# Performance work log

Hardware: AMD Instinct MI355X
Metric: run time of the kernel (lower is better)

The kernel has to match this reference:

```python
import jax, jax.numpy as jnp
import numpy as np

N_NODES = 100000
N_EDGES = 1600000
IN_DIM = 64
EMBED_DIM = 128
OUT_DIM = 10


def setup_inputs() -> dict:
    key = jax.random.key(0)
    ks = jax.random.split(key, 12)
    x = jax.random.normal(ks[0], (N_NODES, IN_DIM), dtype=jnp.float32)
    edge_index = jax.random.randint(ks[1], (2, N_EDGES), 0, N_NODES, dtype=jnp.int64)
    s = lambda k, shp, fan_in: jax.random.normal(k, shp, dtype=jnp.float32) / np.sqrt(fan_in)
    # SAGEConv params: lin_l (applied to aggregated neighbors, has bias), lin_r (root, no bias)
    W_l = s(ks[2], (IN_DIM, EMBED_DIM), IN_DIM)
    b_l = jnp.zeros((EMBED_DIM,), dtype=jnp.float32)
    W_r = s(ks[3], (IN_DIM, EMBED_DIM), IN_DIM)
    # Classifier MLP: embed -> 64 -> 128 -> out
    W1 = s(ks[4], (EMBED_DIM, 64), EMBED_DIM)
    b1 = jnp.zeros((64,), dtype=jnp.float32)
    W2 = s(ks[5], (64, 128), 64)
    b2 = jnp.zeros((128,), dtype=jnp.float32)
    W3 = s(ks[6], (128, OUT_DIM), 128)
    b3 = jnp.zeros((OUT_DIM,), dtype=jnp.float32)
    return {"x": x, "edge_index": edge_index, "W_l": W_l, "b_l": b_l, "W_r": W_r,
            "W1": W1, "b1": b1, "W2": W2, "b2": b2, "W3": W3, "b3": b3}


def reference(x, edge_index, W_l, b_l, W_r, W1, b1, W2, b2, W3, b3):
    src, dst = edge_index[0], edge_index[1]
    # mean-aggregate neighbor features: gather x[src], scatter-sum to dst, divide by degree
    msg = x[src]                                                   # [E, in_dim]
    agg = jax.ops.segment_sum(msg, dst, num_segments=N_NODES)      # [N, in_dim]
    deg = jax.ops.segment_sum(jnp.ones((src.shape[0],), x.dtype), dst, num_segments=N_NODES)
    mean = agg / jnp.maximum(deg, 1.0)[:, None]                    # [N, in_dim]
    # SAGEConv: lin_l(mean_neigh) + lin_r(x_root)
    h = mean @ W_l + b_l + x @ W_r                                 # [N, embed_dim]
    # classifier MLP (logits)
    h = jax.nn.relu(h @ W1 + b1)
    h = jax.nn.relu(h @ W2 + b2)
    return h @ W3 + b3
```

## Files before the change

kernel.cpp:

```cpp
#include <hip/hip_runtime.h>
#include <hip/hip_bf16.h>

#define N_NODES 100000
#define IN_DIM 64
#define EMB 128
#define HID1 64
#define HID2 128
#define OUT_DIM 10

#define CHUNK 8192
#define NBUCK ((N_NODES + 511) >> 9)
#define CAPB 9216

using short8 = __attribute__((ext_vector_type(8))) short;
using bfx4   = __attribute__((ext_vector_type(4))) short;
using f32x4  = __attribute__((ext_vector_type(4))) float;

__device__ inline short f2bf(float f) {
  __hip_bfloat16 h = __float2bfloat16(f);
  return *reinterpret_cast<short*>(&h);
}

#define WCAT_N (128 * 128)
#define W1T_N  (64 * 128)
#define W2T_N  (128 * 64)
#define W3T_N  (16 * 128)
__global__ __launch_bounds__(256) void prep_weights(
    const float* __restrict__ W_l, const float* __restrict__ W_r,
    const float* __restrict__ W1, const float* __restrict__ W2,
    const float* __restrict__ W3,
    short* __restrict__ wcat_t, short* __restrict__ w1t,
    short* __restrict__ w2t, short* __restrict__ w3t)
{
  int t = blockIdx.x * 256 + threadIdx.x;
  if (t < WCAT_N) {
    int c = t >> 7, k = t & 127;
    float v = (k < 64) ? W_r[k * EMB + c] : W_l[(k - 64) * EMB + c];
    wcat_t[c * 128 + k] = f2bf(v);
  } else if (t < WCAT_N + W1T_N) {
    int u = t - WCAT_N;
    int c = u >> 7, k = u & 127;
    w1t[c * 128 + k] = f2bf(W1[k * HID1 + c]);
  } else if (t < WCAT_N + W1T_N + W2T_N) {
    int u = t - WCAT_N - W1T_N;
    int c = u >> 6, k = u & 63;
    w2t[c * 64 + k] = f2bf(W2[k * HID2 + c]);
  } else if (t < WCAT_N + W1T_N + W2T_N + W3T_N) {
    int u = t - WCAT_N - W1T_N - W2T_N;
    int c = u >> 7, k = u & 127;
    w3t[c * 128 + k] = (c < OUT_DIM) ? f2bf(W3[k * OUT_DIM + c]) : (short)0;
  }
}

__global__ __launch_bounds__(256) void convert_x(
    const float* __restrict__ x, short* __restrict__ comb)
{
  int t = blockIdx.x * 256 + threadIdx.x;
  if (t >= N_NODES * 16) return;
  int node = t >> 4, g = t & 15;
  f32x4 v = *(const f32x4*)&x[(size_t)node * IN_DIM + g * 4];
  bfx4 s;
#pragma unroll
  for (int i = 0; i < 4; ++i) s[i] = f2bf(v[i]);
  *(bfx4*)&comb[((size_t)node << 7) + g * 4] = s;
}

__global__ __launch_bounds__(256) void bin_scatter(
    const int* __restrict__ src, const int* __restrict__ dst,
    int* __restrict__ gcur, int* __restrict__ ebuf, int E)
{
  __shared__ int hist[NBUCK], excl[NBUCK], cur[NBUCK], gb[NBUCK];
  __shared__ int stage[CHUNK];
  __shared__ unsigned char bof[CHUNK];
  __shared__ int sc[256];
  const int tid = threadIdx.x;
  const int base = blockIdx.x * CHUNK;
  const int cn = min(CHUNK, E - base);

  for (int i = tid; i < NBUCK; i += 256) hist[i] = 0;
  __syncthreads();
  for (int i = tid; i < cn; i += 256) atomicAdd(&hist[dst[base + i] >> 9], 1);
  __syncthreads();

  int v = (tid < NBUCK) ? hist[tid] : 0;
  sc[tid] = v;
  __syncthreads();
  for (int off = 1; off < 256; off <<= 1) {
    int u = (tid >= off) ? sc[tid - off] : 0;
    __syncthreads();
    sc[tid] += u;
    __syncthreads();
  }
  if (tid < NBUCK) {
    int ex = sc[tid] - v;
    excl[tid] = ex; cur[tid] = ex;
    gb[tid] = v ? atomicAdd(&gcur[tid], v) : 0;
  }
  __syncthreads();

  for (int i = tid; i < cn; i += 256) {
    int d = dst[base + i], s = src[base + i];
    int bk = d >> 9;
    int pos = atomicAdd(&cur[bk], 1);
    stage[pos] = ((d & 511) << 17) | s;
    bof[pos] = (unsigned char)bk;
  }
  __syncthreads();

  for (int i = tid; i < cn; i += 256) {
    int bk = bof[i];
    int idx = gb[bk] + (i - excl[bk]);
    if (idx < CAPB) ebuf[bk * CAPB + idx] = stage[i];
  }
}

__global__ __launch_bounds__(256) void bucket_csr(
    const int* __restrict__ gcur, int* __restrict__ ebuf,
    int* __restrict__ offs, int* __restrict__ oend)
{
  __shared__ int cnt[512], cur[512], sc[512];
  __shared__ int ep[CAPB];
  __shared__ int es[CAPB];
  const int b = blockIdx.x, tid = threadIdx.x;
  const int node0 = b << 9;
  const int nn = min(512, N_NODES - node0);
  const int ebase = b * CAPB;
  const int ecnt = min(gcur[b], CAPB);

  for (int i = tid; i < 512; i += 256) cnt[i] = 0;
  __syncthreads();
  for (int i = tid; i < ecnt; i += 256) {
    int p = ebuf[ebase + i];
    ep[i] = p;
    atomicAdd(&cnt[p >> 17], 1);
  }
  __syncthreads();
  for (int i = tid; i < 512; i += 256) sc[i] = cnt[i];
  __syncthreads();
  for (int off = 1; off < 512; off <<= 1) {
    int i0 = tid, i1 = tid + 256;
    int v0 = (i0 >= off) ? sc[i0 - off] : 0;
    int v1 = (i1 >= off) ? sc[i1 - off] : 0;
    __syncthreads();
    sc[i0] += v0; sc[i1] += v1;
    __syncthreads();
  }
  for (int i = tid; i < 512; i += 256) {
    int ex = sc[i] - cnt[i];
    cur[i] = ex;
    if (i < nn) {
      offs[node0 + i] = ebase + ex;
      oend[node0 + i] = ebase + sc[i];
    }
  }
  __syncthreads();
  for (int i = tid; i < ecnt; i += 256) {
    int p = ep[i];
    int pos = atomicAdd(&cur[p >> 17], 1);
    es[pos] = p & 131071;
  }
  __syncthreads();
  for (int i = tid; i < ecnt; i += 256) ebuf[ebase + i] = es[i];
}

__global__ __launch_bounds__(256) void aggregate_kernel(
    const int* __restrict__ offs, const int* __restrict__ oend,
    const int* __restrict__ esrc, short* __restrict__ comb)
{
  int wave = (int)((blockIdx.x * 256 + threadIdx.x) >> 6);
  int lane = threadIdx.x & 63;
  if (wave >= N_NODES) return;
  const int h = lane >> 5, li = lane & 31;
  const int beg = offs[wave], end = oend[wave];
  float a0 = 0.f, a1 = 0.f;

  for (int e = beg; e < end; e += 64) {
    const int cnt = min(end - e, 64);
    int sidx = (lane < cnt) ? esrc[e + lane] : 0;
    int jb = 0;
    for (; jb + 16 <= cnt; jb += 16) {
      int j = jb + h;
      int s0 = __shfl(sidx, j,      64);
      int s1 = __shfl(sidx, j + 2,  64);
      int s2 = __shfl(sidx, j + 4,  64);
      int s3 = __shfl(sidx, j + 6,  64);
      int s4 = __shfl(sidx, j + 8,  64);
      int s5 = __shfl(sidx, j + 10, 64);
      int s6 = __shfl(sidx, j + 12, 64);
      int s7 = __shfl(sidx, j + 14, 64);
      unsigned v0 = *(const unsigned*)&comb[((size_t)s0 << 7) + (li << 1)];
      unsigned v1 = *(const unsigned*)&comb[((size_t)s1 << 7) + (li << 1)];
      unsigned v2 = *(const unsigned*)&comb[((size_t)s2 << 7) + (li << 1)];
      unsigned v3 = *(const unsigned*)&comb[((size_t)s3 << 7) + (li << 1)];
      unsigned v4 = *(const unsigned*)&comb[((size_t)s4 << 7) + (li << 1)];
      unsigned v5 = *(const unsigned*)&comb[((size_t)s5 << 7) + (li << 1)];
      unsigned v6 = *(const unsigned*)&comb[((size_t)s6 << 7) + (li << 1)];
      unsigned v7 = *(const unsigned*)&comb[((size_t)s7 << 7) + (li << 1)];
      a0 += __uint_as_float(v0 << 16); a1 += __uint_as_float(v0 & 0xFFFF0000u);
      a0 += __uint_as_float(v1 << 16); a1 += __uint_as_float(v1 & 0xFFFF0000u);
      a0 += __uint_as_float(v2 << 16); a1 += __uint_as_float(v2 & 0xFFFF0000u);
      a0 += __uint_as_float(v3 << 16); a1 += __uint_as_float(v3 & 0xFFFF0000u);
      a0 += __uint_as_float(v4 << 16); a1 += __uint_as_float(v4 & 0xFFFF0000u);
      a0 += __uint_as_float(v5 << 16); a1 += __uint_as_float(v5 & 0xFFFF0000u);
      a0 += __uint_as_float(v6 << 16); a1 += __uint_as_float(v6 & 0xFFFF0000u);
      a0 += __uint_as_float(v7 << 16); a1 += __uint_as_float(v7 & 0xFFFF0000u);
    }
    if (jb + 8 <= cnt) {
      int j = jb + h;
      int s0 = __shfl(sidx, j,     64);
      int s1 = __shfl(sidx, j + 2, 64);
      int s2 = __shfl(sidx, j + 4, 64);
      int s3 = __shfl(sidx, j + 6, 64);
      unsigned v0 = *(const unsigned*)&comb[((size_t)s0 << 7) + (li << 1)];
      unsigned v1 = *(const unsigned*)&comb[((size_t)s1 << 7) + (li << 1)];
      unsigned v2 = *(const unsigned*)&comb[((size_t)s2 << 7) + (li << 1)];
      unsigned v3 = *(const unsigned*)&comb[((size_t)s3 << 7) + (li << 1)];
      a0 += __uint_as_float(v0 << 16); a1 += __uint_as_float(v0 & 0xFFFF0000u);
      a0 += __uint_as_float(v1 << 16); a1 += __uint_as_float(v1 & 0xFFFF0000u);
      a0 += __uint_as_float(v2 << 16); a1 += __uint_as_float(v2 & 0xFFFF0000u);
      a0 += __uint_as_float(v3 << 16); a1 += __uint_as_float(v3 & 0xFFFF0000u);
      jb += 8;
    }
    for (; jb < cnt; jb += 2) {
      int j = jb + h;
      int s0 = __shfl(sidx, j & 63, 64);
      if (j < cnt) {
        unsigned v0 = *(const unsigned*)&comb[((size_t)s0 << 7) + (li << 1)];
        a0 += __uint_as_float(v0 << 16); a1 += __uint_as_float(v0 & 0xFFFF0000u);
      }
    }
  }
  a0 += __shfl_xor(a0, 32, 64);
  a1 += __shfl_xor(a1, 32, 64);
  if (h == 0) {
    float d = fmaxf((float)(end - beg), 1.0f);
    float m0 = a0 / d, m1 = a1 / d;
    unsigned p = ((unsigned)(unsigned short)f2bf(m1) << 16) |
                 (unsigned short)f2bf(m0);
    *(unsigned*)&comb[((size_t)wave << 7) + 64 + (li << 1)] = p;
  }
}

#define PA 128
#define PH 64

__global__ __launch_bounds__(256) void fused_mfma_kernel(
    const short* __restrict__ comb,
    const short* __restrict__ wcat_t, const short* __restrict__ w1t,
    const short* __restrict__ w2t, const short* __restrict__ w3t,
    const float* __restrict__ b_l, const float* __restrict__ b1,
    const float* __restrict__ b2, const float* __restrict__ b3,
    float* __restrict__ out)
{
  __shared__ __align__(16) short sA0[64 * PA];
  __shared__ __align__(16) short sH [64 * PA];
  __shared__ __align__(16) short sH1[64 * PH];
  __shared__ __align__(16) short sW [128 * PA];

  const int tid  = threadIdx.x;
  const int base = blockIdx.x * 64;
  const int lane = tid & 63;
  const int w    = tid >> 6;
  const int lrow = lane & 15;
  const int lgrp = lane >> 4;

  for (int T = tid; T < 1024; T += 256) {
    int n = T >> 4, g = T & 15;
    int node = base + n;
    short8 s = {0, 0, 0, 0, 0, 0, 0, 0};
    if (node < N_NODES) s = *(const short8*)&comb[(size_t)node * 128 + 8 * g];
    *(short8*)&sA0[(n * PA + 8 * g) ^ ((n & 7) << 3)] = s;
  }
  for (int T = tid; T < 2048; T += 256) {
    int c = T >> 4, kg = T & 15;
    *(short8*)&sW[(c * PA + 8 * kg) ^ ((c & 7) << 3)] =
        *(const short8*)&wcat_t[c * 128 + 8 * kg];
  }
  __syncthreads();

  {
    const int c0w = 32 * w;
    short8 bf[2][4];
#pragma unroll
    for (int ct = 0; ct < 2; ++ct)
#pragma unroll
      for (int kk = 0; kk < 4; ++kk) {
        int row = c0w + 16 * ct + lrow;
        bf[ct][kk] = *(const short8*)&sW[(row * PA + kk * 32 + lgrp * 8) ^ ((row & 7) << 3)];
      }
#pragma unroll
    for (int rt = 0; rt < 4; ++rt) {
      short8 af[4];
#pragma unroll
      for (int kk = 0; kk < 4; ++kk) {
        int row = rt * 16 + lrow;
        af[kk] = *(const short8*)&sA0[(row * PA + kk * 32 + lgrp * 8) ^ ((row & 7) << 3)];
      }
#pragma unroll
      for (int ct = 0; ct < 2; ++ct) {
        float bv = b_l[c0w + 16 * ct + lrow];
        f32x4 acc = {bv, bv, bv, bv};
#pragma unroll
        for (int kk = 0; kk < 4; ++kk)
          acc = __builtin_amdgcn_mfma_f32_16x16x32_bf16(af[kk], bf[ct][kk], acc, 0, 0, 0);
        int col = c0w + 16 * ct + lrow;
        int rb = rt * 16 + lgrp * 4;
#pragma unroll
        for (int r = 0; r < 4; ++r) {
          int row = rb + r;
          sH[(row * PA + col) ^ ((row & 7) << 3)] = f2bf(acc[r]);
        }
      }
    }
  }
  __syncthreads();

  for (int T = tid; T < 1024; T += 256) {
    int c = T >> 4, kg = T & 15;
    *(short8*)&sW[(c * PA + 8 * kg) ^ ((c & 7) << 3)] =
        *(const short8*)&w1t[c * 128 + 8 * kg];
  }
  {
    int c = tid >> 4, kg = tid & 15;
    *(short8*)&sA0[(c * PA + 8 * kg) ^ ((c & 7) << 3)] =
        *(const short8*)&w3t[c * 128 + 8 * kg];
  }
  __syncthreads();

  {
    const int c0 = 16 * w;
    short8 bf[4];
#pragma unroll
    for (int kk = 0; kk < 4; ++kk) {
      int row = c0 + lrow;
      bf[kk] = *(const short8*)&sW[(row * PA + kk * 32 + lgrp * 8) ^ ((row & 7) << 3)];
    }
#pragma unroll
    for (int rt = 0; rt < 4; ++rt) {
      short8 af[4];
#pragma unroll
      for (int kk = 0; kk < 4; ++kk) {
        int row = rt * 16 + lrow;
        af[kk] = *(const short8*)&sH[(row * PA + kk * 32 + lgrp * 8) ^ ((row & 7) << 3)];
      }
      float bv = b1[c0 + lrow];
      f32x4 acc = {bv, bv, bv, bv};
#pragma unroll
      for (int kk = 0; kk < 4; ++kk)
        acc = __builtin_amdgcn_mfma_f32_16x16x32_bf16(af[kk], bf[kk], acc, 0, 0, 0);
      int col = c0 + lrow;
      int rb = rt * 16 + lgrp * 4;
#pragma unroll
      for (int r = 0; r < 4; ++r) {
        int row = rb + r;
        sH1[(row * PH + col) ^ ((row & 7) << 3)] = f2bf(fmaxf(acc[r], 0.f));
      }
    }
  }
  __syncthreads();

  for (int T = tid; T < 1024; T += 256) {
    int c = T >> 3, kg = T & 7;
    *(short8*)&sW[(c * PA + 8 * kg) ^ ((c & 7) << 3)] =
        *(const short8*)&w2t[c * 64 + 8 * kg];
  }
  __syncthreads();

  {
    const int c0w = 32 * w;
    short8 bf[2][2];
#pragma unroll
    for (int ct = 0; ct < 2; ++ct)
#pragma unroll
      for (int kk = 0; kk < 2; ++kk) {
        int row = c0w + 16 * ct + lrow;
        bf[ct][kk] = *(const short8*)&sW[(row * PA + kk * 32 + lgrp * 8) ^ ((row & 7) << 3)];
      }
#pragma unroll
    for (int rt = 0; rt < 4; ++rt) {
      short8 af[2];
#pragma unroll
      for (int kk = 0; kk < 2; ++kk) {
        int row = rt * 16 + lrow;
        af[kk] = *(const short8*)&sH1[(row * PH + kk * 32 + lgrp * 8) ^ ((row & 7) << 3)];
      }
#pragma unroll
      for (int ct = 0; ct < 2; ++ct) {
        float bv = b2[c0w + 16 * ct + lrow];
        f32x4 acc = {bv, bv, bv, bv};
#pragma unroll
        for (int kk = 0; kk < 2; ++kk)
          acc = __builtin_amdgcn_mfma_f32_16x16x32_bf16(af[kk], bf[ct][kk], acc, 0, 0, 0);
        int col = c0w + 16 * ct + lrow;
        int rb = rt * 16 + lgrp * 4;
#pragma unroll
        for (int r = 0; r < 4; ++r) {
          int row = rb + r;
          sH[(row * PA + col) ^ ((row & 7) << 3)] = f2bf(fmaxf(acc[r], 0.f));
        }
      }
    }
  }
  __syncthreads();

  {
    short8 af[4], bf[4];
#pragma unroll
    for (int kk = 0; kk < 4; ++kk) {
      int row = 16 * w + lrow;
      af[kk] = *(const short8*)&sH[(row * PA + kk * 32 + lgrp * 8) ^ ((row & 7) << 3)];
      bf[kk] = *(const short8*)&sA0[(lrow * PA + kk * 32 + lgrp * 8) ^ ((lrow & 7) << 3)];
    }
    float bv = (lrow < OUT_DIM) ? b3[lrow] : 0.f;
    f32x4 acc = {bv, bv, bv, bv};
#pragma unroll
    for (int kk = 0; kk < 4; ++kk)
      acc = __builtin_amdgcn_mfma_f32_16x16x32_bf16(af[kk], bf[kk], acc, 0, 0, 0);
#pragma unroll
    for (int r = 0; r < 4; ++r) {
      int row = 16 * w + lgrp * 4 + r;
      int node = base + row;
      if (node < N_NODES && lrow < OUT_DIM)
        out[(long long)node * OUT_DIM + lrow] = acc[r];
    }
  }
}

extern "C" void kernel_launch(void* const* d_in, const int* in_sizes, int n_in,
                              void* d_out, int out_size, void* d_ws, size_t ws_size,
                              hipStream_t stream) {
  const float* x   = (const float*)d_in[0];
  const int*   ei  = (const int*)d_in[1];
  const float* W_l = (const float*)d_in[2];
  const float* b_l = (const float*)d_in[3];
  const float* W_r = (const float*)d_in[4];
  const float* W1  = (const float*)d_in[5];
  const float* b1  = (const float*)d_in[6];
  const float* W2  = (const float*)d_in[7];
  const float* b2  = (const float*)d_in[8];
  const float* W3  = (const float*)d_in[9];
  const float* b3  = (const float*)d_in[10];
  float* out = (float*)d_out;

  const int E = in_sizes[1] / 2;
  const int* src = ei;
  const int* dst = ei + E;

  short* wcat_t = (short*)d_ws;
  short* w1t    = wcat_t + WCAT_N;
  short* w2t    = w1t + W1T_N;
  short* w3t    = w2t + W2T_N;
  short* comb   = w3t + W3T_N;
  int*   offs   = (int*)(comb + (size_t)N_NODES * 128);
  int*   oend   = offs + N_NODES;
  int*   ebuf   = oend + N_NODES;
  int*   gcur   = ebuf + (size_t)NBUCK * CAPB;

  (void)hipMemsetAsync(gcur, 0, NBUCK * sizeof(int), stream);

  int nbW = (WCAT_N + W1T_N + W2T_N + W3T_N + 255) / 256;
  prep_weights<<<nbW, 256, 0, stream>>>(W_l, W_r, W1, W2, W3, wcat_t, w1t, w2t, w3t);

  int nbX = (N_NODES * 16 + 255) / 256;
  convert_x<<<nbX, 256, 0, stream>>>(x, comb);

  const int nbC = (E + CHUNK - 1) / CHUNK;
  bin_scatter<<<nbC, 256, 0, stream>>>(src, dst, gcur, ebuf, E);
  bucket_csr<<<NBUCK, 256, 0, stream>>>(gcur, ebuf, offs, oend);

  int nbAgg = (N_NODES * 64 + 255) / 256;
  aggregate_kernel<<<nbAgg, 256, 0, stream>>>(offs, oend, ebuf, comb);

  int nbF = (N_NODES + 63) / 64;
  fused_mfma_kernel<<<nbF, 256, 0, stream>>>(comb, wcat_t, w1t, w2t, w3t,
                                             b_l, b1, b2, b3, out);
}
```

Baseline: 129.5 us.

## Merge front-end kernels into one launch and simplify per-node aggregation

Weight prep, x-to-bf16 conversion and edge binning now run as branches of one kernel chosen by block index, which drops two launches and lets these independent jobs share the GPU at once. The aggregation kernel now gives each lane one feature column of a node. It reads edge indices as wave-uniform scalar loads instead of shuffles and unrolls by 16/8/4. This removes shuffle and half-wave bookkeeping but issues 2-byte gathers per lane instead of 4-byte ones. The combined kernel also reserves the binning branch's large shared-memory footprint for the conversion and weight-prep blocks, which may lower their occupancy.

```diff
diff --git a/kernel.cpp b/kernel.cpp
--- a/kernel.cpp
+++ b/kernel.cpp
@@ -12,105 +12,112 @@
 #define NBUCK ((N_NODES + 511) >> 9)
 #define CAPB 9216
 
-using short8 = __attribute__((ext_vector_type(8))) short;
-using bfx4   = __attribute__((ext_vector_type(4))) short;
-using f32x4  = __attribute__((ext_vector_type(4))) float;
-
-__device__ inline short f2bf(float f) {
-  __hip_bfloat16 h = __float2bfloat16(f);
-  return *reinterpret_cast<short*>(&h);
-}
-
+#define NB_CONV ((N_NODES * 16) / 256)
 #define WCAT_N (128 * 128)
 #define W1T_N  (64 * 128)
 #define W2T_N  (128 * 64)
 #define W3T_N  (16 * 128)
-__global__ __launch_bounds__(256) void prep_weights(
+#define PREP_TOT (WCAT_N + W1T_N + W2T_N + W3T_N)
+#define NB_PREP ((PREP_TOT + 255) / 256)
+
+using short8 = __attribute__((ext_vector_type(8))) short;
+using bfx4   = __attribute__((ext_vector_type(4))) short;
+using f32x4  = __attribute__((ext_vector_type(4))) float;
+
+__device__ inline short f2bf(float f) {
+  __hip_bfloat16 h = __float2bfloat16(f);
+  return *reinterpret_cast<short*>(&h);
+}
+
+struct BinShared {
+  int hist[NBUCK], excl[NBUCK], cur[NBUCK], gb[NBUCK];
+  int stage[CHUNK];
+  unsigned char bof[CHUNK];
+  int sc[256];
+};
+
+__global__ __launch_bounds__(256) void frontend_kernel(
+    const float* __restrict__ x,
+    const int* __restrict__ src, const int* __restrict__ dst,
     const float* __restrict__ W_l, const float* __restrict__ W_r,
     const float* __restrict__ W1, const float* __restrict__ W2,
     const float* __restrict__ W3,
+    int* __restrict__ gcur, int* __restrict__ ebuf, short* __restrict__ comb,
     short* __restrict__ wcat_t, short* __restrict__ w1t,
-    short* __restrict__ w2t, short* __restrict__ w3t)
+    short* __restrict__ w2t, short* __restrict__ w3t,
+    int E, int nbC)
 {
-  int t = blockIdx.x * 256 + threadIdx.x;
-  if (t < WCAT_N) {
-    int c = t >> 7, k = t & 127;
-    float v = (k < 64) ? W_r[k * EMB + c] : W_l[(k - 64) * EMB + c];
-    wcat_t[c * 128 + k] = f2bf(v);
-  } else if (t < WCAT_N + W1T_N) {
-    int u = t - WCAT_N;
-    int c = u >> 7, k = u & 127;
-    w1t[c * 128 + k] = f2bf(W1[k * HID1 + c]);
-  } else if (t < WCAT_N + W1T_N + W2T_N) {
-    int u = t - WCAT_N - W1T_N;
-    int c = u >> 6, k = u & 63;
-    w2t[c * 64 + k] = f2bf(W2[k * HID2 + c]);
-  } else if (t < WCAT_N + W1T_N + W2T_N + W3T_N) {
-    int u = t - WCAT_N - W1T_N - W2T_N;
-    int c = u >> 7, k = u & 127;
-    w3t[c * 128 + k] = (c < OUT_DIM) ? f2bf(W3[k * OUT_DIM + c]) : (short)0;
-  }
-}
-
-__global__ __launch_bounds__(256) void convert_x(
-    const float* __restrict__ x, short* __restrict__ comb)
-{
-  int t = blockIdx.x * 256 + threadIdx.x;
-  if (t >= N_NODES * 16) return;
-  int node = t >> 4, g = t & 15;
-  f32x4 v = *(const f32x4*)&x[(size_t)node * IN_DIM + g * 4];
-  bfx4 s;
-#pragma unroll
-  for (int i = 0; i < 4; ++i) s[i] = f2bf(v[i]);
-  *(bfx4*)&comb[((size_t)node << 7) + g * 4] = s;
-}
-
-__global__ __launch_bounds__(256) void bin_scatter(
-    const int* __restrict__ src, const int* __restrict__ dst,
-    int* __restrict__ gcur, int* __restrict__ ebuf, int E)
-{
-  __shared__ int hist[NBUCK], excl[NBUCK], cur[NBUCK], gb[NBUCK];
-  __shared__ int stage[CHUNK];
-  __shared__ unsigned char bof[CHUNK];
-  __shared__ int sc[256];
+  __shared__ __align__(16) char smem_raw[sizeof(BinShared)];
+  const int b = blockIdx.x;
   const int tid = threadIdx.x;
-  const int base = blockIdx.x * CHUNK;
-  const int cn = min(CHUNK, E - base);
-
-  for (int i = tid; i < NBUCK; i += 256) hist[i] = 0;
-  __syncthreads();
-  for (int i = tid; i < cn; i += 256) atomicAdd(&hist[dst[base + i] >> 9], 1);
-  __syncthreads();
-
-  int v = (tid < NBUCK) ? hist[tid] : 0;
-  sc[tid] = v;
-  __syncthreads();
-  for (int off = 1; off < 256; off <<= 1) {
-    int u = (tid >= off) ? sc[tid - off] : 0;
-    __syncthreads();
-    sc[tid] += u;
-    __syncthreads();
-  }
-  if (tid < NBUCK) {
-    int ex = sc[tid] - v;
-    excl[tid] = ex; cur[tid] = ex;
-    gb[tid] = v ? atomicAdd(&gcur[tid], v) : 0;
-  }
-  __syncthreads();
-
-  for (int i = tid; i < cn; i += 256) {
-    int d = dst[base + i], s = src[base + i];
-    int bk = d >> 9;
-    int pos = atomicAdd(&cur[bk], 1);
-    stage[pos] = ((d & 511) << 17) | s;
-    bof[pos] = (unsigned char)bk;
-  }
-  __syncthreads();
-
-  for (int i = tid; i < cn; i += 256) {
-    int bk = bof[i];
-    int idx = gb[bk] + (i - excl[bk]);
-    if (idx < CAPB) ebuf[bk * CAPB + idx] = stage[i];
+
+  if (b < nbC) {
+    BinShared& S = *reinterpret_cast<BinShared*>(smem_raw);
+    const int base = b * CHUNK;
+    const int cn = min(CHUNK, E - base);
+
+    for (int i = tid; i < NBUCK; i += 256) S.hist[i] = 0;
+    __syncthreads();
+    for (int i = tid; i < cn; i += 256) atomicAdd(&S.hist[dst[base + i] >> 9], 1);
+    __syncthreads();
+
+    int v = (tid < NBUCK) ? S.hist[tid] : 0;
+    S.sc[tid] = v;
+    __syncthreads();
+    for (int off = 1; off < 256; off <<= 1) {
+      int u = (tid >= off) ? S.sc[tid - off] : 0;
+      __syncthreads();
+      S.sc[tid] += u;
+      __syncthreads();
+    }
+    if (tid < NBUCK) {
+      int ex = S.sc[tid] - v;
+      S.excl[tid] = ex; S.cur[tid] = ex;
+      S.gb[tid] = v ? atomicAdd(&gcur[tid], v) : 0;
+    }
+    __syncthreads();
+
+    for (int i = tid; i < cn; i += 256) {
+      int d = dst[base + i], s = src[base + i];
+      int bk = d >> 9;
+      int pos = atomicAdd(&S.cur[bk], 1);
+      S.stage[pos] = ((d & 511) << 17) | s;
+      S.bof[pos] = (unsigned char)bk;
+    }
+    __syncthreads();
+
+    for (int i = tid; i < cn; i += 256) {
+      int bk = S.bof[i];
+      int idx = S.gb[bk] + (i - S.excl[bk]);
+      if (idx < CAPB) ebuf[bk * CAPB + idx] = S.stage[i];
+    }
+  } else if (b < nbC + NB_CONV) {
+    int t = (b - nbC) * 256 + tid;
+    int node = t >> 4, g = t & 15;
+    f32x4 v = *(const f32x4*)&x[(size_t)node * IN_DIM + g * 4];
+    bfx4 s;
+#pragma unroll
+    for (int i = 0; i < 4; ++i) s[i] = f2bf(v[i]);
+    *(bfx4*)&comb[((size_t)node << 7) + g * 4] = s;
+  } else {
+    int t = (b - nbC - NB_CONV) * 256 + tid;
+    if (t < WCAT_N) {
+      int c = t >> 7, k = t & 127;
+      float v = (k < 64) ? W_r[k * EMB + c] : W_l[(k - 64) * EMB + c];
+      wcat_t[c * 128 + k] = f2bf(v);
+    } else if (t < WCAT_N + W1T_N) {
+      int u = t - WCAT_N;
+      int c = u >> 7, k = u & 127;
+      w1t[c * 128 + k] = f2bf(W1[k * HID1 + c]);
+    } else if (t < WCAT_N + W1T_N + W2T_N) {
+      int u = t - WCAT_N - W1T_N;
+      int c = u >> 6, k = u & 63;
+      w2t[c * 64 + k] = f2bf(W2[k * HID2 + c]);
+    } else if (t < PREP_TOT) {
+      int u = t - WCAT_N - W1T_N - W2T_N;
+      int c = u >> 7, k = u & 127;
+      w3t[c * 128 + k] = (c < OUT_DIM) ? f2bf(W3[k * OUT_DIM + c]) : (short)0;
+    }
   }
 }
 
@@ -167,78 +174,82 @@
     const int* __restrict__ offs, const int* __restrict__ oend,
     const int* __restrict__ esrc, short* __restrict__ comb)
 {
-  int wave = (int)((blockIdx.x * 256 + threadIdx.x) >> 6);
-  int lane = threadIdx.x & 63;
-  if (wave >= N_NODES) return;
-  const int h = lane >> 5, li = lane & 31;
-  const int beg = offs[wave], end = oend[wave];
-  float a0 = 0.f, a1 = 0.f;
-
-  for (int e = beg; e < end; e += 64) {
-    const int cnt = min(end - e, 64);
-    int sidx = (lane < cnt) ? esrc[e + lane] : 0;
-    int jb = 0;
-    for (; jb + 16 <= cnt; jb += 16) {
-      int j = jb + h;
-      int s0 = __shfl(sidx, j,      64);
-      int s1 = __shfl(sidx, j + 2,  64);
-      int s2 = __shfl(sidx, j + 4,  64);
-      int s3 = __shfl(sidx, j + 6,  64);
-      int s4 = __shfl(sidx, j + 8,  64);
-      int s5 = __shfl(sidx, j + 10, 64);
-      int s6 = __shfl(sidx, j + 12, 64);
-      int s7 = __shfl(sidx, j + 14, 64);
-      unsigned v0 = *(const unsigned*)&comb[((size_t)s0 << 7) + (li << 1)];
-      unsigned v1 = *(const unsigned*)&comb[((size_t)s1 << 7) + (li << 1)];
-      unsigned v2 = *(const unsigned*)&comb[((size_t)s2 << 7) + (li << 1)];
-      unsigned v3 = *(const unsigned*)&comb[((size_t)s3 << 7) + (li << 1)];
-      unsigned v4 = *(const unsigned*)&comb[((size_t)s4 << 7) + (li << 1)];
-      unsigned v5 = *(const unsigned*)&comb[((size_t)s5 << 7) + (li << 1)];
-      unsigned v6 = *(const unsigned*)&comb[((size_t)s6 << 7) + (li << 1)];
-      unsigned v7 = *(const unsigned*)&comb[((size_t)s7 << 7) + (li << 1)];
-      a0 += __uint_as_float(v0 << 16); a1 += __uint_as_float(v0 & 0xFFFF0000u);
-      a0 += __uint_as_float(v1 << 16); a1 += __uint_as_float(v1 & 0xFFFF0000u);
-      a0 += __uint_as_float(v2 << 16); a1 += __uint_as_float(v2 & 0xFFFF0000u);
-      a0 += __uint_as_float(v3 << 16); a1 += __uint_as_float(v3 & 0xFFFF0000u);
-      a0 += __uint_as_float(v4 << 16); a1 += __uint_as_float(v4 & 0xFFFF0000u);
-      a0 += __uint_as_float(v5 << 16); a1 += __uint_as_float(v5 & 0xFFFF0000u);
-      a0 += __uint_as_float(v6 << 16); a1 += __uint_as_float(v6 & 0xFFFF0000u);
-      a0 += __uint_as_float(v7 << 16); a1 += __uint_as_float(v7 & 0xFFFF0000u);
-    }
-    if (jb + 8 <= cnt) {
-      int j = jb + h;
-      int s0 = __shfl(sidx, j,     64);
-      int s1 = __shfl(sidx, j + 2, 64);
-      int s2 = __shfl(sidx, j + 4, 64);
-      int s3 = __shfl(sidx, j + 6, 64);
-      unsigned v0 = *(const unsigned*)&comb[((size_t)s0 << 7) + (li << 1)];
-      unsigned v1 = *(const unsigned*)&comb[((size_t)s1 << 7) + (li << 1)];
-      unsigned v2 = *(const unsigned*)&comb[((size_t)s2 << 7) + (li << 1)];
-      unsigned v3 = *(const unsigned*)&comb[((size_t)s3 << 7) + (li << 1)];
-      a0 += __uint_as_float(v0 << 16); a1 += __uint_as_float(v0 & 0xFFFF0000u);
-      a0 += __uint_as_float(v1 << 16); a1 += __uint_as_float(v1 & 0xFFFF0000u);
-      a0 += __uint_as_float(v2 << 16); a1 += __uint_as_float(v2 & 0xFFFF0000u);
-      a0 += __uint_as_float(v3 << 16); a1 += __uint_as_float(v3 & 0xFFFF0000u);
-      jb += 8;
-    }
-    for (; jb < cnt; jb += 2) {
-      int j = jb + h;
-      int s0 = __shfl(sidx, j & 63, 64);
-      if (j < cnt) {
-        unsigned v0 = *(const unsigned*)&comb[((size_t)s0 << 7) + (li << 1)];
-        a0 += __uint_as_float(v0 << 16); a1 += __uint_as_float(v0 & 0xFFFF0000u);
-      }
-    }
-  }
-  a0 += __shfl_xor(a0, 32, 64);
-  a1 += __shfl_xor(a1, 32, 64);
-  if (h == 0) {
-    float d = fmaxf((float)(end - beg), 1.0f);
-    float m0 = a0 / d, m1 = a1 / d;
-    unsigned p = ((unsigned)(unsigned short)f2bf(m1) << 16) |
-                 (unsigned short)f2bf(m0);
-    *(unsigned*)&comb[((size_t)wave << 7) + 64 + (li << 1)] = p;
-  }
+  int wv = (int)((blockIdx.x * 256 + threadIdx.x) >> 6);
+  const int lane = threadIdx.x & 63;
+  const int node = __builtin_amdgcn_readfirstlane(wv);
+  if (node >= N_NODES) return;
+  const int beg = offs[node];
+  const int end = oend[node];
+  const int deg = end - beg;
+  const unsigned short* cb = (const unsigned short*)comb;
+  float a = 0.f;
+
+  int k = beg;
+  for (; k + 16 <= end; k += 16) {
+    unsigned o0  = ((unsigned)esrc[k]      << 7) + lane;
+    unsigned o1  = ((unsigned)esrc[k + 1]  << 7) + lane;
+    unsigned o2  = ((unsigned)esrc[k + 2]  << 7) + lane;
+    unsigned o3  = ((unsigned)esrc[k + 3]  << 7) + lane;
+    unsigned o4  = ((unsigned)esrc[k + 4]  << 7) + lane;
+    unsigned o5  = ((unsigned)esrc[k + 5]  << 7) + lane;
+    unsigned o6  = ((unsigned)esrc[k + 6]  << 7) + lane;
+    unsigned o7  = ((unsigned)esrc[k + 7]  << 7) + lane;
+    unsigned o8  = ((unsigned)esrc[k + 8]  << 7) + lane;
+    unsigned o9  = ((unsigned)esrc[k + 9]  << 7) + lane;
+    unsigned o10 = ((unsigned)esrc[k + 10] << 7) + lane;
+    unsigned o11 = ((unsigned)esrc[k + 11] << 7) + lane;
+    unsigned o12 = ((unsigned)esrc[k + 12] << 7) + lane;
+    unsigned o13 = ((unsigned)esrc[k + 13] << 7) + lane;
+    unsigned o14 = ((unsigned)esrc[k + 14] << 7) + lane;
+    unsigned o15 = ((unsigned)esrc[k + 15] << 7) + lane;
+    unsigned u0  = cb[o0],  u1  = cb[o1],  u2  = cb[o2],  u3  = cb[o3];
+    unsigned u4  = cb[o4],  u5  = cb[o5],  u6  = cb[o6],  u7  = cb[o7];
+    unsigned u8  = cb[o8],  u9  = cb[o9],  u10 = cb[o10], u11 = cb[o11];
+    unsigned u12 = cb[o12], u13 = cb[o13], u14 = cb[o14], u15 = cb[o15];
+    a += __uint_as_float(u0  << 16); a += __uint_as_float(u1  << 16);
+    a += __uint_as_float(u2  << 16); a += __uint_as_float(u3  << 16);
+    a += __uint_as_float(u4  << 16); a += __uint_as_float(u5  << 16);
+    a += __uint_as_float(u6  << 16); a += __uint_as_float(u7  << 16);
+    a += __uint_as_float(u8  << 16); a += __uint_as_float(u9  << 16);
+    a += __uint_as_float(u10 << 16); a += __uint_as_float(u11 << 16);
+    a += __uint_as_float(u12 << 16); a += __uint_as_float(u13 << 16);
+    a += __uint_as_float(u14 << 16); a += __uint_as_float(u15 << 16);
+  }
+  if (k + 8 <= end) {
+    unsigned o0 = ((unsigned)esrc[k]     << 7) + lane;
+    unsigned o1 = ((unsigned)esrc[k + 1] << 7) + lane;
+    unsigned o2 = ((unsigned)esrc[k + 2] << 7) + lane;
+    unsigned o3 = ((unsigned)esrc[k + 3] << 7) + lane;
+    unsigned o4 = ((unsigned)esrc[k + 4] << 7) + lane;
+    unsigned o5 = ((unsigned)esrc[k + 5] << 7) + lane;
+    unsigned o6 = ((unsigned)esrc[k + 6] << 7) + lane;
+    unsigned o7 = ((unsigned)esrc[k + 7] << 7) + lane;
+    unsigned u0 = cb[o0], u1 = cb[o1], u2 = cb[o2], u3 = cb[o3];
+    unsigned u4 = cb[o4], u5 = cb[o5], u6 = cb[o6], u7 = cb[o7];
+    a += __uint_as_float(u0 << 16); a += __uint_as_float(u1 << 16);
+    a += __uint_as_float(u2 << 16); a += __uint_as_float(u3 << 16);
+    a += __uint_as_float(u4 << 16); a += __uint_as_float(u5 << 16);
+    a += __uint_as_float(u6 << 16); a += __uint_as_float(u7 << 16);
+    k += 8;
+  }
+  if (k + 4 <= end) {
+    unsigned o0 = ((unsigned)esrc[k]     << 7) + lane;
+    unsigned o1 = ((unsigned)esrc[k + 1] << 7) + lane;
+    unsigned o2 = ((unsigned)esrc[k + 2] << 7) + lane;
+    unsigned o3 = ((unsigned)esrc[k + 3] << 7) + lane;
+    unsigned u0 = cb[o0], u1 = cb[o1], u2 = cb[o2], u3 = cb[o3];
+    a += __uint_as_float(u0 << 16); a += __uint_as_float(u1 << 16);
+    a += __uint_as_float(u2 << 16); a += __uint_as_float(u3 << 16);
+    k += 4;
+  }
+  for (; k < end; ++k) {
+    unsigned u0 = cb[((unsigned)esrc[k] << 7) + lane];
+    a += __uint_as_float(u0 << 16);
+  }
+
+  float m = a / fmaxf((float)deg, 1.0f);
+  ((unsigned short*)comb)[((size_t)node << 7) + 64 + lane] =
+      (unsigned short)f2bf(m);
 }
 
 #define PA 128
@@ -458,14 +469,11 @@
 
   (void)hipMemsetAsync(gcur, 0, NBUCK * sizeof(int), stream);
 
-  int nbW = (WCAT_N + W1T_N + W2T_N + W3T_N + 255) / 256;
-  prep_weights<<<nbW, 256, 0, stream>>>(W_l, W_r, W1, W2, W3, wcat_t, w1t, w2t, w3t);
-
-  int nbX = (N_NODES * 16 + 255) / 256;
-  convert_x<<<nbX, 256, 0, stream>>>(x, comb);
-
   const int nbC = (E + CHUNK - 1) / CHUNK;
-  bin_scatter<<<nbC, 256, 0, stream>>>(src, dst, gcur, ebuf, E);
+  frontend_kernel<<<nbC + NB_CONV + NB_PREP, 256, 0, stream>>>(
+      x, src, dst, W_l, W_r, W1, W2, W3,
+      gcur, ebuf, comb, wcat_t, w1t, w2t, w3t, E, nbC);
+
   bucket_csr<<<NBUCK, 256, 0, stream>>>(gcur, ebuf, offs, oend);
 
   int nbAgg = (N_NODES * 64 + 255) / 256;
```

New measurement: 118.1 us. 1.1x faster.
